# Optimization experiments

Measured on AMD Instinct MI355X. Metric: run time of the kernel, lower is better.

## Reference

```python
import jax, jax.numpy as jnp
import numpy as np
import math

SCALE = 16.0
IGNORE_THRES = 0.5
BAD_CONF_WEIGHT = 1.25
NB, NT, NA, NH, NW, NC = 16, 50, 5, 128, 128, 20


def _inv_tanh(y):
    ys = jnp.clip(y, -1.0 + 1e-6, 1.0 - 1e-6)
    at = 0.5 * jnp.log((1.0 + ys) / (1.0 - ys))
    return jnp.where(y <= -1.0, -2.0, jnp.where(y >= 1.0, 2.0, at))


def _forward(prediction, target, target_sizes, anchors):
    nB, nA, nH, nW, _ = prediction.shape
    nC = prediction.shape[-1] - 6
    s = SCALE
    # scaled anchors and anchor corner points (matches __init__ precompute)
    aw = anchors[:, 0] / s
    ah = anchors[:, 1] / s
    ar = anchors[:, 2]
    cr, sr = jnp.cos(ar), jnp.sin(ar)
    anchor_points = jnp.stack([-cr * aw, sr * aw, cr * aw, -sr * aw,
                               -sr * ah, -cr * ah, sr * ah, cr * ah], axis=1)  # [nA,8]
    anchor_hws = (ah + aw) / 2.0

    pred_conf = prediction[..., 0]
    x = prediction[..., 1]; y = prediction[..., 2]; r = prediction[..., 3]
    h = prediction[..., 4]; w = prediction[..., 5]
    pred_cls = prediction[..., 6:]

    # ---- build_targets_dist, vectorized (original uses detached .cpu().data) ----
    tgt = jax.lax.stop_gradient(target)
    T = tgt.shape[1]
    valid = jnp.arange(T)[None, :] < target_sizes[:, None]
    gx = tgt[..., 0] / s; gy = tgt[..., 1] / s
    gw = tgt[..., 4] / s; gh = tgt[..., 3] / s
    gr = tgt[..., 2]
    valid = valid & (gw != 0) & (gh != 0)
    gi = jnp.clip(gx.astype(jnp.int32), 0, nW - 1)
    gj = jnp.clip(gy.astype(jnp.int32), 0, nH - 1)
    pts = tgt[..., 5:13] / s
    cpts = pts - jnp.tile(jnp.stack([gx, gy], axis=-1), (1, 1, 4))  # centered corners [nB,T,8]
    deltas = cpts[:, :, None, :] - anchor_points[None, None, :, :]  # [nB,T,nA,8]
    dn = sum(jnp.linalg.norm(deltas[..., i:i + 2], axis=-1) for i in (0, 2, 4, 6))
    norm = (((gh + gw) / 2.0)[:, :, None] + anchor_hws[None, None, :]) / 2.0
    anch_dists = (dn / norm) ** 2  # [nB,T,nA]

    # conf_mask: zero anchors closer than ignore_thres at (gj,gi)
    conf_mask = jnp.ones((nB, nA, nH, nW), jnp.float32)
    b3 = jnp.broadcast_to(jnp.arange(nB)[:, None, None], (nB, T, nA)).reshape(-1)
    a3 = jnp.broadcast_to(jnp.arange(nA)[None, None, :], (nB, T, nA)).reshape(-1)
    gj3 = jnp.broadcast_to(gj[:, :, None], (nB, T, nA)).reshape(-1)
    gi3 = jnp.broadcast_to(gi[:, :, None], (nB, T, nA)).reshape(-1)
    ign = ((anch_dists < IGNORE_THRES) & valid[:, :, None]).reshape(-1)
    conf_mask = conf_mask.at[b3, a3, gj3, gi3].min(jnp.where(ign, 0.0, 1.0))

    best_n = jnp.argmin(anch_dists, axis=-1)  # [nB,T]
    txv = _inv_tanh(gx - (gi.astype(jnp.float32) + 0.5))
    tyv = _inv_tanh(gy - (gj.astype(jnp.float32) + 0.5))
    rd = gr - ar[best_n]
    rd = jnp.where(rd > math.pi, rd - 2 * math.pi,
                   jnp.where(rd < -math.pi, rd + 2 * math.pi, rd))
    trv = _inv_tanh(rd / (math.pi / 2))
    twv = jnp.log(gw / aw[best_n] + 1e-16)
    thv = jnp.log(gh / ah[best_n] + 1e-16)
    tlabv = jnp.argmax(tgt[..., 13:], axis=-1)

    bS = jnp.where(valid, jnp.arange(nB)[:, None], -1).reshape(-1)  # -1 -> dropped
    idx = (bS, best_n.reshape(-1), gj.reshape(-1), gi.reshape(-1))
    z = jnp.zeros((nB, nA, nH, nW), jnp.float32)
    mask = z.at[idx].set(1.0, mode='drop')
    conf_mask = conf_mask.at[idx].set(1.0, mode='drop')
    tx = z.at[idx].set(txv.reshape(-1), mode='drop')
    ty = z.at[idx].set(tyv.reshape(-1), mode='drop')
    tw = z.at[idx].set(twv.reshape(-1), mode='drop')
    th = z.at[idx].set(thv.reshape(-1), mode='drop')
    tr = z.at[idx].set(trv.reshape(-1), mode='drop')
    tconf = mask  # tconf set to 1 exactly where mask is 1
    tlab = jnp.zeros((nB, nA, nH, nW), jnp.int32).at[idx].set(
        tlabv.reshape(-1).astype(jnp.int32), mode='drop')

    conf_mask_false = conf_mask * (1.0 - mask)

    def masked_bce(z_, t_, m_):
        l = jnp.maximum(z_, 0.0) - z_ * t_ + jnp.log1p(jnp.exp(-jnp.abs(z_)))
        return jnp.sum(l * m_) / jnp.maximum(jnp.sum(m_), 1.0)

    def masked_mse(p_, t_):
        return jnp.sum(((p_ - t_) ** 2) * mask) / jnp.maximum(jnp.sum(mask), 1.0)

    loss_conf = BAD_CONF_WEIGHT * masked_bce(pred_conf, tconf, conf_mask_false) \
        + masked_bce(pred_conf, tconf, mask)
    loss_x = masked_mse(x, tx); loss_y = masked_mse(y, ty)
    loss_w = masked_mse(w, tw); loss_h = masked_mse(h, th)
    loss_r = masked_mse(r, tr)
    logp = jax.nn.log_softmax(pred_cls, axis=-1)
    nll = -jnp.take_along_axis(logp, tlab[..., None], axis=-1)[..., 0]
    loss_cls = jnp.sum(nll * mask) / jnp.maximum(jnp.sum(mask), 1.0)
    return loss_x + loss_y + loss_w + loss_h + loss_r + loss_conf + loss_cls


def setup_inputs():
    key = jax.random.key(0)
    ks = jax.random.split(key, 8)
    s = SCALE
    prediction = jax.random.normal(ks[0], (NB, NA, NH, NW, 6 + NC), jnp.float32) * 0.5
    # targets in image pixel space (grid is NHxNW at stride SCALE)
    cx = jax.random.uniform(ks[1], (NB, NT), minval=1.0, maxval=NW - 1.0) * s
    cy = jax.random.uniform(ks[2], (NB, NT), minval=1.0, maxval=NH - 1.0) * s
    bw = jax.random.uniform(ks[3], (NB, NT), minval=8.0, maxval=96.0)
    bh = jax.random.uniform(ks[4], (NB, NT), minval=8.0, maxval=48.0)
    br = jax.random.uniform(ks[5], (NB, NT), minval=-0.3, maxval=0.3)
    c, si = jnp.cos(br), jnp.sin(br)
    pts = jnp.stack([cx - c * bw, cy + si * bw, cx + c * bw, cy - si * bw,
                     cx - si * bh, cy - c * bh, cx + si * bh, cy + c * bh], axis=-1)
    cls = jax.nn.one_hot(jax.random.randint(ks[6], (NB, NT), 0, NC), NC, dtype=jnp.float32)
    target = jnp.concatenate([jnp.stack([cx, cy, br, bh, bw], axis=-1), pts, cls], axis=-1)
    target_sizes = jax.random.randint(ks[7], (NB,), 20, NT + 1).astype(jnp.int32)
    anchors = jnp.array([[48., 16., 0.], [96., 24., 0.], [192., 32., 0.],
                         [64., 64., 0.], [32., 96., 1.5708]], jnp.float32)
    return {"prediction": prediction, "target": target,
            "target_sizes": target_sizes, "anchors": anchors}


def reference(prediction, target, target_sizes, anchors):
    return _forward(prediction, target, target_sizes, anchors)
```

## Files before the change

### kernel.cpp

```cpp
#include <hip/hip_runtime.h>
#include <math.h>

#define NBb 16
#define NTt 50
#define NAa 5
#define NHh 128
#define NWw 128
#define NCc 20
#define NCH 26
#define NCELL (NBb*NAa*NHh*NWw)
#define NFLAT (NCELL*NCH)
#define NQ4   (NFLAT/4)
#define NREC  (NBb*NTt)
#define NLIST (NREC*7)
#define SCALE_F 16.0f
#define IGNORE_THRES_F 0.5f
#define BAD_CONF_WEIGHT_F 1.25f
#define PI_F 3.14159265358979323846f

#define STATUS_OFF 16
#define REC_OFF  (STATUS_OFF + NCELL)
#define LIST_OFF (REC_OFF + 6*NREC)

__device__ __forceinline__ float inv_tanh_f(float y) {
  if (y <= -1.0f) return -2.0f;
  if (y >= 1.0f)  return  2.0f;
  float ys = fminf(fmaxf(y, -1.0f + 1e-6f), 1.0f - 1e-6f);
  return 0.5f * logf((1.0f + ys) / (1.0f - ys));
}

__device__ __forceinline__ float softplus_f(float z) {
  return fmaxf(z, 0.0f) + log1pf(expf(-fabsf(z)));
}

__global__ void k_zero(unsigned* __restrict__ wsu) {
  int stride = gridDim.x * blockDim.x;
  for (int i = blockIdx.x * blockDim.x + threadIdx.x;
       i < STATUS_OFF + NCELL; i += stride)
    wsu[i] = 0u;
}

__global__ void k_prep(const float* __restrict__ tgt,
                       const int* __restrict__ tsz,
                       const float* __restrict__ anch,
                       float* __restrict__ ws) {
  int tid = blockIdx.x * blockDim.x + threadIdx.x;
  if (tid >= NREC) return;
  int b = tid / NTt, t = tid % NTt;

  float aw[NAa], ah[NAa], ar[NAa], ahw[NAa], ap[NAa][8];
  for (int a = 0; a < NAa; ++a) {
    aw[a] = anch[a*3+0] / SCALE_F;
    ah[a] = anch[a*3+1] / SCALE_F;
    ar[a] = anch[a*3+2];
    float cr = cosf(ar[a]), sr = sinf(ar[a]);
    ap[a][0] = -cr*aw[a]; ap[a][1] =  sr*aw[a];
    ap[a][2] =  cr*aw[a]; ap[a][3] = -sr*aw[a];
    ap[a][4] = -sr*ah[a]; ap[a][5] = -cr*ah[a];
    ap[a][6] =  sr*ah[a]; ap[a][7] =  cr*ah[a];
    ahw[a] = (ah[a] + aw[a]) * 0.5f;
  }

  const float* row = tgt + (size_t)tid * (13 + NCc);
  float gx = row[0] / SCALE_F;
  float gy = row[1] / SCALE_F;
  float gr = row[2];
  float gh = row[3] / SCALE_F;
  float gw = row[4] / SCALE_F;
  bool valid = (t < tsz[b]) && (gw != 0.0f) && (gh != 0.0f);
  if (!valid) return;

  int gi = (int)gx; gi = min(max(gi, 0), NWw - 1);
  int gj = (int)gy; gj = min(max(gj, 0), NHh - 1);

  float cp[8];
  for (int k = 0; k < 8; ++k)
    cp[k] = row[5 + k] / SCALE_F - ((k & 1) ? gy : gx);

  float bestd = 1e30f; int best = 0; unsigned ignm = 0;
  for (int a = 0; a < NAa; ++a) {
    float dn = 0.0f;
    for (int p = 0; p < 8; p += 2) {
      float dx = cp[p]   - ap[a][p];
      float dy = cp[p+1] - ap[a][p+1];
      dn += sqrtf(dx*dx + dy*dy);
    }
    float nm = ((gh + gw) * 0.5f + ahw[a]) * 0.5f;
    float d = dn / nm; d = d * d;
    if (d < IGNORE_THRES_F) ignm |= (1u << a);
    if (d < bestd) { bestd = d; best = a; }
  }

  unsigned* wsu = (unsigned*)ws;
  unsigned* status = wsu + STATUS_OFF;
  unsigned* list = wsu + LIST_OFF;
  int cellbase = ((b * NAa) * NHh + gj) * NWw + gi;
  for (int a = 0; a < NAa; ++a)
    if ((ignm >> a) & 1u) {
      int cell = cellbase + a * NHh * NWw;
      atomicMax(&status[cell], 1u);
      unsigned slot = atomicAdd(&wsu[15], 1u);
      list[slot] = (unsigned)cell;
    }
  {
    int cell = cellbase + best * NHh * NWw;
    atomicMax(&status[cell], 2u + (unsigned)tid);
    if (!((ignm >> best) & 1u)) {
      unsigned slot = atomicAdd(&wsu[15], 1u);
      list[slot] = (unsigned)cell;
    }
  }

  float txv = inv_tanh_f(gx - ((float)gi + 0.5f));
  float tyv = inv_tanh_f(gy - ((float)gj + 0.5f));
  float rd = gr - ar[best];
  if (rd > PI_F) rd -= 2.0f * PI_F;
  else if (rd < -PI_F) rd += 2.0f * PI_F;
  float trv = inv_tanh_f(rd / (PI_F * 0.5f));
  float twv = logf(gw / aw[best] + 1e-16f);
  float thv = logf(gh / ah[best] + 1e-16f);
  int tlab = 0; float bm = row[13];
  for (int c = 1; c < NCc; ++c)
    if (row[13 + c] > bm) { bm = row[13 + c]; tlab = c; }

  float* rec = ws + REC_OFF;
  rec[0*NREC + tid] = txv;
  rec[1*NREC + tid] = tyv;
  rec[2*NREC + tid] = twv;
  rec[3*NREC + tid] = thv;
  rec[4*NREC + tid] = trv;
  ((int*)rec)[5*NREC + tid] = tlab;
}

__global__ void k_sum(const float4* __restrict__ pred4, float* __restrict__ ws) {
  float acc = 0.0f;
  int stride = gridDim.x * blockDim.x;
  for (int q = blockIdx.x * blockDim.x + threadIdx.x; q < NQ4; q += stride) {
    float4 v = pred4[q];
    int m13 = q % 13;
    if (m13 == 0)      acc += softplus_f(v.x);
    else if (m13 == 6) acc += softplus_f(v.z);
  }
  for (int off = 32; off; off >>= 1) acc += __shfl_down(acc, off, 64);
  __shared__ float s0[8];
  int wid = threadIdx.x >> 6, lane = threadIdx.x & 63;
  if (lane == 0) s0[wid] = acc;
  __syncthreads();
  if (threadIdx.x == 0) {
    float a = 0.0f;
    int nw = blockDim.x >> 6;
    for (int w = 0; w < nw; ++w) a += s0[w];
    atomicAdd(ws + 0, a);
  }
}

__global__ void __launch_bounds__(1024) k_fixfin(const float* __restrict__ pred,
                                                 float* __restrict__ ws,
                                                 float* __restrict__ out) {
  unsigned* wsu = (unsigned*)ws;
  unsigned* status = wsu + STATUS_OFF;
  const unsigned* list = wsu + LIST_OFF;
  const float* rec = ws + REC_OFF;
  int nlist = (int)wsu[15];

  float sub = 0.0f, cnb = 0.0f, obj = 0.0f;
  float sx = 0.0f, sy = 0.0f, sw = 0.0f, sh = 0.0f, sr = 0.0f;
  float scls = 0.0f, cm = 0.0f;

  for (int i = threadIdx.x; i < nlist; i += 1024) {
    unsigned cell = list[i];
    unsigned st = atomicExch(&status[cell], 0u);
    if (st == 0u) continue;
    const float* cp = pred + (size_t)cell * NCH;
    float z = cp[0];
    sub += softplus_f(z);
    cnb += 1.0f;
    if (st >= 2u) {
      int r = (int)(st - 2u);
      obj += softplus_f(z) - z;
      float dx = cp[1] - rec[0*NREC + r];
      float dy = cp[2] - rec[1*NREC + r];
      float dr = cp[3] - rec[4*NREC + r];
      float dh = cp[4] - rec[3*NREC + r];
      float dw = cp[5] - rec[2*NREC + r];
      sx += dx*dx; sy += dy*dy; sw += dw*dw; sh += dh*dh; sr += dr*dr;
      int tlab = ((const int*)rec)[5*NREC + r];
      float m = cp[6];
      for (int c = 1; c < NCc; ++c) m = fmaxf(m, cp[6 + c]);
      float s = 0.0f;
      for (int c = 0; c < NCc; ++c) s += expf(cp[6 + c] - m);
      scls += (m + logf(s)) - cp[6 + tlab];
      cm += 1.0f;
    }
  }

  float vals[10] = {sub, cnb, obj, sx, sy, sw, sh, sr, scls, cm};
  __shared__ float red[16][10];
  int wid = threadIdx.x >> 6, lane = threadIdx.x & 63;
  for (int k = 0; k < 10; ++k) {
    float v = vals[k];
    for (int off = 32; off; off >>= 1) v += __shfl_down(v, off, 64);
    if (lane == 0) red[wid][k] = v;
    vals[k] = v;
  }
  __syncthreads();
  if (threadIdx.x == 0) {
    float tot[10];
    for (int k = 0; k < 10; ++k) {
      float v = 0.0f;
      for (int w = 0; w < 16; ++w) v += red[w][k];
      tot[k] = v;
    }
    float acc_bg = ws[0] - tot[0];
    float cnt_bg = (float)NCELL - tot[1];
    float db = fmaxf(cnt_bg, 1.0f);
    float dm = fmaxf(tot[9], 1.0f);
    float loss_conf = BAD_CONF_WEIGHT_F * (acc_bg / db) + tot[2] / dm;
    out[0] = (tot[3] + tot[4] + tot[5] + tot[6] + tot[7] + tot[8]) / dm + loss_conf;
  }
}

extern "C" void kernel_launch(void* const* d_in, const int* in_sizes, int n_in,
                              void* d_out, int out_size, void* d_ws, size_t ws_size,
                              hipStream_t stream) {
  const float* pred = (const float*)d_in[0];
  const float* tgt  = (const float*)d_in[1];
  const int*   tsz  = (const int*)d_in[2];
  const float* anch = (const float*)d_in[3];
  float* ws = (float*)d_ws;

  k_zero<<<1280, 256, 0, stream>>>((unsigned*)ws);
  k_prep<<<4, 256, 0, stream>>>(tgt, tsz, anch, ws);
  k_sum<<<4096, 256, 0, stream>>>((const float4*)pred, ws);
  k_fixfin<<<1, 1024, 0, stream>>>(pred, ws, (float*)d_out);
}
```

Baseline: 243.4 us.

## Replace global status array with shared-memory hash dedup, drop zeroing kernel

Removes the 1.3M-entry global status array and its zeroing kernel. k_prep now emits (cell, value) pairs and clears the counters itself in a single block. The final kernel deduplicates cells with an open-addressing hash table in LDS using atomicCAS and atomicMax. The main sum kernel also switches to nontemporal vector loads. The aim is to cut the memset traffic and one launch, at the cost of a single-block hash build and the assumption that the pair count fits 8192 slots.

```diff
diff --git a/kernel.cpp b/kernel.cpp
--- a/kernel.cpp
+++ b/kernel.cpp
@@ -12,14 +12,16 @@
 #define NFLAT (NCELL*NCH)
 #define NQ4   (NFLAT/4)
 #define NREC  (NBb*NTt)
-#define NLIST (NREC*7)
 #define SCALE_F 16.0f
 #define IGNORE_THRES_F 0.5f
 #define BAD_CONF_WEIGHT_F 1.25f
 #define PI_F 3.14159265358979323846f
-
-#define STATUS_OFF 16
-#define REC_OFF  (STATUS_OFF + NCELL)
+#define HSLOTS 8192
+#define HEMPTY 0xFFFFFFFFu
+
+typedef float __attribute__((ext_vector_type(4))) fvec4;
+
+#define REC_OFF  16
 #define LIST_OFF (REC_OFF + 6*NREC)
 
 __device__ __forceinline__ float inv_tanh_f(float y) {
@@ -33,18 +35,14 @@
   return fmaxf(z, 0.0f) + log1pf(expf(-fabsf(z)));
 }
 
-__global__ void k_zero(unsigned* __restrict__ wsu) {
-  int stride = gridDim.x * blockDim.x;
-  for (int i = blockIdx.x * blockDim.x + threadIdx.x;
-       i < STATUS_OFF + NCELL; i += stride)
-    wsu[i] = 0u;
-}
-
-__global__ void k_prep(const float* __restrict__ tgt,
-                       const int* __restrict__ tsz,
-                       const float* __restrict__ anch,
-                       float* __restrict__ ws) {
-  int tid = blockIdx.x * blockDim.x + threadIdx.x;
+__global__ void __launch_bounds__(1024) k_prep(const float* __restrict__ tgt,
+                                               const int* __restrict__ tsz,
+                                               const float* __restrict__ anch,
+                                               float* __restrict__ ws) {
+  unsigned* wsu = (unsigned*)ws;
+  if (threadIdx.x < 16) wsu[threadIdx.x] = 0u;
+  __syncthreads();
+  int tid = threadIdx.x;
   if (tid >= NREC) return;
   int b = tid / NTt, t = tid % NTt;
 
@@ -91,24 +89,18 @@
     if (d < bestd) { bestd = d; best = a; }
   }
 
-  unsigned* wsu = (unsigned*)ws;
-  unsigned* status = wsu + STATUS_OFF;
   unsigned* list = wsu + LIST_OFF;
   int cellbase = ((b * NAa) * NHh + gj) * NWw + gi;
   for (int a = 0; a < NAa; ++a)
     if ((ignm >> a) & 1u) {
-      int cell = cellbase + a * NHh * NWw;
-      atomicMax(&status[cell], 1u);
       unsigned slot = atomicAdd(&wsu[15], 1u);
-      list[slot] = (unsigned)cell;
+      list[2*slot]   = (unsigned)(cellbase + a * NHh * NWw);
+      list[2*slot+1] = 1u;
     }
   {
-    int cell = cellbase + best * NHh * NWw;
-    atomicMax(&status[cell], 2u + (unsigned)tid);
-    if (!((ignm >> best) & 1u)) {
-      unsigned slot = atomicAdd(&wsu[15], 1u);
-      list[slot] = (unsigned)cell;
-    }
+    unsigned slot = atomicAdd(&wsu[15], 1u);
+    list[2*slot]   = (unsigned)(cellbase + best * NHh * NWw);
+    list[2*slot+1] = 2u + (unsigned)tid;
   }
 
   float txv = inv_tanh_f(gx - ((float)gi + 0.5f));
@@ -132,11 +124,11 @@
   ((int*)rec)[5*NREC + tid] = tlab;
 }
 
-__global__ void k_sum(const float4* __restrict__ pred4, float* __restrict__ ws) {
+__global__ void k_sum(const fvec4* __restrict__ pred4, float* __restrict__ ws) {
   float acc = 0.0f;
   int stride = gridDim.x * blockDim.x;
   for (int q = blockIdx.x * blockDim.x + threadIdx.x; q < NQ4; q += stride) {
-    float4 v = pred4[q];
+    fvec4 v = __builtin_nontemporal_load(&pred4[q]);
     int m13 = q % 13;
     if (m13 == 0)      acc += softplus_f(v.x);
     else if (m13 == 6) acc += softplus_f(v.z);
@@ -158,19 +150,36 @@
                                                  float* __restrict__ ws,
                                                  float* __restrict__ out) {
   unsigned* wsu = (unsigned*)ws;
-  unsigned* status = wsu + STATUS_OFF;
   const unsigned* list = wsu + LIST_OFF;
   const float* rec = ws + REC_OFF;
-  int nlist = (int)wsu[15];
+  int npair = (int)wsu[15];
+
+  __shared__ unsigned hkey[HSLOTS];
+  __shared__ unsigned hval[HSLOTS];
+  for (int s = threadIdx.x; s < HSLOTS; s += 1024) {
+    hkey[s] = HEMPTY; hval[s] = 0u;
+  }
+  __syncthreads();
+
+  for (int i = threadIdx.x; i < npair; i += 1024) {
+    unsigned cell = list[2*i], v = list[2*i+1];
+    unsigned s = (cell * 2654435761u) >> 19;
+    for (;;) {
+      unsigned k = atomicCAS(&hkey[s], HEMPTY, cell);
+      if (k == HEMPTY || k == cell) { atomicMax(&hval[s], v); break; }
+      s = (s + 1) & (HSLOTS - 1);
+    }
+  }
+  __syncthreads();
 
   float sub = 0.0f, cnb = 0.0f, obj = 0.0f;
   float sx = 0.0f, sy = 0.0f, sw = 0.0f, sh = 0.0f, sr = 0.0f;
   float scls = 0.0f, cm = 0.0f;
 
-  for (int i = threadIdx.x; i < nlist; i += 1024) {
-    unsigned cell = list[i];
-    unsigned st = atomicExch(&status[cell], 0u);
-    if (st == 0u) continue;
+  for (int s = threadIdx.x; s < HSLOTS; s += 1024) {
+    unsigned cell = hkey[s];
+    if (cell == HEMPTY) continue;
+    unsigned st = hval[s];
     const float* cp = pred + (size_t)cell * NCH;
     float z = cp[0];
     sub += softplus_f(z);
@@ -187,9 +196,9 @@
       int tlab = ((const int*)rec)[5*NREC + r];
       float m = cp[6];
       for (int c = 1; c < NCc; ++c) m = fmaxf(m, cp[6 + c]);
-      float s = 0.0f;
-      for (int c = 0; c < NCc; ++c) s += expf(cp[6 + c] - m);
-      scls += (m + logf(s)) - cp[6 + tlab];
+      float s2 = 0.0f;
+      for (int c = 0; c < NCc; ++c) s2 += expf(cp[6 + c] - m);
+      scls += (m + logf(s2)) - cp[6 + tlab];
       cm += 1.0f;
     }
   }
@@ -201,7 +210,6 @@
     float v = vals[k];
     for (int off = 32; off; off >>= 1) v += __shfl_down(v, off, 64);
     if (lane == 0) red[wid][k] = v;
-    vals[k] = v;
   }
   __syncthreads();
   if (threadIdx.x == 0) {
@@ -229,8 +237,7 @@
   const float* anch = (const float*)d_in[3];
   float* ws = (float*)d_ws;
 
-  k_zero<<<1280, 256, 0, stream>>>((unsigned*)ws);
-  k_prep<<<4, 256, 0, stream>>>(tgt, tsz, anch, ws);
-  k_sum<<<4096, 256, 0, stream>>>((const float4*)pred, ws);
+  k_prep<<<1, 1024, 0, stream>>>(tgt, tsz, anch, ws);
+  k_sum<<<4096, 256, 0, stream>>>((const fvec4*)pred, ws);
   k_fixfin<<<1, 1024, 0, stream>>>(pred, ws, (float*)d_out);
 }
```

New measurement: 282.5 us. +16.1%, slower.
